# Performance work log

Measured on AMD Instinct MI355X. Metric: run time of the kernel, lower is better.

## Reference

```python
import jax, jax.numpy as jnp
import numpy as np

N = 50000; E = 800000; H = 4; C = 64; FEAT = 128; EDIM = 16; G = 256
NEG_SLOPE = 0.2; BN_EPS = 1e-5


def _gat_layer(x, src, dst, W, a_src, a_dst, bias, gamma, beta, alpha_edge=None):
    # GATConv (concat=True, PyG math), then BatchNorm1d (batch stats) + ReLU.
    h = (x @ W).reshape(N, H, C)                       # [N,H,C]
    alpha = (h * a_src).sum(-1)[src] + (h * a_dst).sum(-1)[dst]   # [Etot,H]
    if alpha_edge is not None:
        alpha = alpha + alpha_edge
    alpha = jax.nn.leaky_relu(alpha, NEG_SLOPE)
    amax = jax.ops.segment_max(alpha, dst, num_segments=N)        # edge softmax over dst
    ea = jnp.exp(alpha - amax[dst])
    denom = jax.ops.segment_sum(ea, dst, num_segments=N)
    coef = ea / (denom[dst] + 1e-16)
    out = jax.ops.segment_sum(coef[:, :, None] * h[src], dst, num_segments=N)
    out = out.reshape(N, H * C) + bias
    mu = out.mean(0)
    var = out.var(0)
    out = (out - mu) / jnp.sqrt(var + BN_EPS) * gamma + beta
    return jax.nn.relu(out)


def setup_inputs() -> dict:
    key = jax.random.key(0)
    ks = jax.random.split(key, 32)
    s = 0.05
    inp = {
        "x": jax.random.normal(ks[0], (N, FEAT), jnp.float32),
        "edge_index": jax.random.randint(ks[1], (2, E), 0, N),
        "edge_attr": jax.random.normal(ks[2], (E, EDIM), jnp.float32),
        "batch": jnp.sort(jax.random.randint(ks[3], (N,), 0, G)),
    }
    in_dims = [FEAT, H * C, H * C]
    for i in range(3):
        k = 4 + 7 * i
        inp[f"W{i}"] = jax.random.normal(ks[k], (in_dims[i], H * C), jnp.float32) * s
        inp[f"att_src{i}"] = jax.random.normal(ks[k + 1], (H, C), jnp.float32) * s
        inp[f"att_dst{i}"] = jax.random.normal(ks[k + 2], (H, C), jnp.float32) * s
        inp[f"bias{i}"] = jnp.zeros((H * C,), jnp.float32)
        inp[f"gamma{i}"] = jnp.ones((H * C,), jnp.float32)
        inp[f"beta{i}"] = jnp.zeros((H * C,), jnp.float32)
    inp["We0"] = jax.random.normal(ks[28], (EDIM, H * C), jnp.float32) * s
    inp["att_e0"] = jax.random.normal(ks[29], (H, C), jnp.float32) * s
    return inp


def reference(x, edge_index, edge_attr, batch,
              W0, att_src0, att_dst0, bias0, gamma0, beta0,
              W1, att_src1, att_dst1, bias1, gamma1, beta1,
              W2, att_src2, att_dst2, bias2, gamma2, beta2,
              We0, att_e0):
    # PyG GATConv adds self-loops; edge_attr for self-loops filled with mean.
    loops = jnp.arange(N)
    src = jnp.concatenate([edge_index[0], loops])
    dst = jnp.concatenate([edge_index[1], loops])
    ea_sl = jnp.concatenate([edge_attr, jnp.broadcast_to(edge_attr.mean(0), (N, EDIM))], 0)
    e = (ea_sl @ We0).reshape(E + N, H, C)
    alpha_e = (e * att_e0).sum(-1)                     # [Etot,H]
    x = _gat_layer(x, src, dst, W0, att_src0, att_dst0, bias0, gamma0, beta0, alpha_e)
    x = _gat_layer(x, src, dst, W1, att_src1, att_dst1, bias1, gamma1, beta1)
    x = _gat_layer(x, src, dst, W2, att_src2, att_dst2, bias2, gamma2, beta2)
    # global_mean_pool
    counts = jax.ops.segment_sum(jnp.ones((N,), x.dtype), batch, num_segments=G)
    sums = jax.ops.segment_sum(x, batch, num_segments=G)
    return sums / jnp.clip(counts, 1.0)[:, None]
```

## Files before the change

### kernel.cpp

```cpp
#include <hip/hip_runtime.h>
#include <math.h>

#define NN 50000
#define NE 800000
#define ET 850000
#define HCC 256
#define GG 256
#define CAP 64
#define NB 16

constexpr int RTILES = 782;
constexpr int G0B    = 512;
constexpr int CSRB   = 416;

constexpr size_t NHC    = (size_t)NN * HCC;
constexpr size_t O_H    = 0;
constexpr size_t O_AGG  = O_H + NHC / 2;
constexpr size_t O_REC  = O_AGG + NHC / 2;
constexpr size_t O_BT0  = O_REC + (size_t)NN * CAP * 4;
constexpr size_t O_BT1  = O_BT0 + 16384;
constexpr size_t O_BT2  = O_BT1 + 32768;
constexpr size_t O_AS   = O_BT2 + 32768;
constexpr size_t O_AD   = O_AS + (size_t)NN * 4;
constexpr size_t O_M    = O_AD + (size_t)NN * 4;
constexpr size_t O_ZERO = O_M + 64;
constexpr size_t O_DEG  = O_ZERO;
constexpr size_t O_SLS  = O_DEG + NN;
constexpr size_t O_PART = O_SLS + 4;
constexpr size_t O_END  = O_PART + 3 * NB * 512;
constexpr size_t ZWORDS = O_END - O_ZERO;
constexpr int    ZBLK   = (int)((ZWORDS / 4 + 255) / 256);
constexpr int    XBLK   = (int)((size_t)NN * 128 / 2048);

typedef __attribute__((ext_vector_type(8))) short bf16x8;
typedef __attribute__((ext_vector_type(4))) float f32x4;

__device__ inline unsigned short f2bf(float f) {
    unsigned int u = __float_as_uint(f);
    unsigned int r = (u + 0x7fffu + ((u >> 16) & 1u)) >> 16;
    return (unsigned short)r;
}
__device__ inline float b2f(unsigned short u) {
    return __uint_as_float(((unsigned int)u) << 16);
}
__device__ inline float bflo(unsigned int u) { return __uint_as_float(u << 16); }
__device__ inline float bfhi(unsigned int u) { return __uint_as_float(u & 0xffff0000u); }

__global__ void prep_kernel(const float* __restrict__ W0, const float* __restrict__ W1,
                            const float* __restrict__ W2,
                            const float* __restrict__ We0, const float* __restrict__ att_e0,
                            unsigned short* __restrict__ Bt0,
                            unsigned short* __restrict__ Bt1,
                            unsigned short* __restrict__ Bt2,
                            float* __restrict__ M, float* __restrict__ zbase,
                            const float* __restrict__ x, unsigned short* __restrict__ xb) {
    int b = blockIdx.x;
    if (b >= 641 + ZBLK) {
        size_t i0 = ((size_t)(b - (641 + ZBLK)) * 256 + threadIdx.x) * 8;
        float4 f1 = *(const float4*)(x + i0);
        float4 f2 = *(const float4*)(x + i0 + 4);
        uint4 o;
        o.x = ((unsigned)f2bf(f1.y) << 16) | f2bf(f1.x);
        o.y = ((unsigned)f2bf(f1.w) << 16) | f2bf(f1.z);
        o.z = ((unsigned)f2bf(f2.y) << 16) | f2bf(f2.x);
        o.w = ((unsigned)f2bf(f2.w) << 16) | f2bf(f2.z);
        *(uint4*)(xb + i0) = o;
        return;
    }
    if (b >= 641) {
        size_t idx = ((size_t)(b - 641) * 256 + threadIdx.x) * 4;
        if (idx < ZWORDS)
            *(float4*)(zbase + idx) = make_float4(0.f, 0.f, 0.f, 0.f);
        return;
    }
    if (b == 640) {
        int t = threadIdx.x;
        if (t < 64) {
            int k = t >> 2, hh = t & 3;
            float s = 0.f;
            for (int c = 0; c < 64; ++c)
                s += We0[k * 256 + hh * 64 + c] * att_e0[hh * 64 + c];
            M[k * 4 + hh] = s;
        }
        return;
    }
    const float* W; unsigned short* Bt; int K, base;
    if (b < 128)      { W = W0; Bt = Bt0; K = 128; base = 0; }
    else if (b < 384) { W = W1; Bt = Bt1; K = 256; base = 128; }
    else              { W = W2; Bt = Bt2; K = 256; base = 384; }
    int idx = (b - base) * 256 + threadIdx.x;
    int n = idx & 255, k = idx >> 8;
    Bt[(size_t)n * K + k] = f2bf(W[(size_t)k * 256 + n]);
}

__global__ __launch_bounds__(512) void g0csr(const unsigned short* __restrict__ Ab,
                                             const unsigned short* __restrict__ Bt,
                                             const float* __restrict__ att_src,
                                             const float* __restrict__ att_dst,
                                             unsigned short* __restrict__ Hout,
                                             float* __restrict__ asA,
                                             float* __restrict__ adA,
                                             const int* __restrict__ srcA,
                                             const int* __restrict__ dstA,
                                             const float* __restrict__ ea,
                                             const float* __restrict__ Mm,
                                             int* __restrict__ deg,
                                             uint4* __restrict__ rec,
                                             float* __restrict__ slsum) {
    constexpr int K   = 128;
    constexpr int KP  = K + 8;
    constexpr int NLD = K / 64;
    __shared__ unsigned short Bs[128][KP];
    __shared__ unsigned short As[2][64][KP];
    __shared__ float prt[8][4];

    int tid = threadIdx.x;
    int wave = tid >> 6, lane = tid & 63;

    if (blockIdx.x >= G0B) {
        int t0 = (int)(blockIdx.x - G0B) * 2048 + tid;
        float a0 = 0.f, a1 = 0.f, a2 = 0.f, a3 = 0.f;
        #pragma unroll
        for (int q = 0; q < 4; ++q) {
            int e = t0 + q * 512;
            if (e < ET) {
                bool real = (e < NE);
                int d = real ? dstA[e] : (e - NE);
                int s = real ? srcA[e] : (e - NE);
                int p = atomicAdd(&deg[d], 1);
                if (p > CAP - 1) p = CAP - 1;
                int slot = d * CAP + p;
                uint4 r;
                r.z = (unsigned)s;
                if (real) {
                    r.w = 0u;
                    const float4* pp = (const float4*)(ea + (size_t)e * 16);
                    float4 va = pp[0], vb = pp[1], vc = pp[2], vd = pp[3];
                    float v[16] = {va.x, va.y, va.z, va.w, vb.x, vb.y, vb.z, vb.w,
                                   vc.x, vc.y, vc.z, vc.w, vd.x, vd.y, vd.z, vd.w};
                    float o0 = 0.f, o1 = 0.f, o2 = 0.f, o3 = 0.f;
                    #pragma unroll
                    for (int k = 0; k < 16; ++k) {
                        float4 m4 = *(const float4*)(Mm + k * 4);
                        o0 = fmaf(v[k], m4.x, o0);
                        o1 = fmaf(v[k], m4.y, o1);
                        o2 = fmaf(v[k], m4.z, o2);
                        o3 = fmaf(v[k], m4.w, o3);
                    }
                    r.x = ((unsigned)f2bf(o1) << 16) | (unsigned)f2bf(o0);
                    r.y = ((unsigned)f2bf(o3) << 16) | (unsigned)f2bf(o2);
                    a0 += o0; a1 += o1; a2 += o2; a3 += o3;
                } else {
                    r.x = 0u; r.y = 0u; r.w = 1u;
                }
                rec[slot] = r;
            }
        }
        #pragma unroll
        for (int off = 32; off; off >>= 1) {
            a0 += __shfl_xor(a0, off);
            a1 += __shfl_xor(a1, off);
            a2 += __shfl_xor(a2, off);
            a3 += __shfl_xor(a3, off);
        }
        if (lane == 0) {
            prt[wave][0] = a0; prt[wave][1] = a1;
            prt[wave][2] = a2; prt[wave][3] = a3;
        }
        __syncthreads();
        if (tid < 4) {
            float s = 0.f;
            #pragma unroll
            for (int w = 0; w < 8; ++w) s += prt[w][tid];
            atomicAdd(&slsum[tid], s);
        }
        return;
    }

    int quad = lane >> 4, l16 = lane & 15;
    int wr = wave >> 1, wc = wave & 1;

    int b = blockIdx.x;
    int cb = (b >> 3) & 1;
    int ts = ((b >> 4) << 3) | (b & 7);
    const int np = G0B >> 1;
    int colbase = cb * 128;
    int head = cb * 2 + wc;

    {
        constexpr int TOT = 128 * K;
        for (int idx = tid * 8; idx < TOT; idx += 4096) {
            int br = idx / K, bk = idx % K;
            uint4 v = *(const uint4*)(Bt + (size_t)(colbase + br) * K + bk);
            *(uint4*)&Bs[br][bk] = v;
        }
    }

    int srow = tid >> 3;
    const int scol0 = (tid & 7) * (K / 8);

    uint4 ldA_[NLD], ldB_[NLD];

    auto issue = [&](uint4 (&ld)[NLD], int t) {
        int r = t * 64 + srow;
        if (r < NN) {
            const uint4* src = (const uint4*)(Ab + (size_t)r * K + scol0);
            #pragma unroll
            for (int q = 0; q < NLD; ++q) ld[q] = src[q];
        } else {
            #pragma unroll
            for (int q = 0; q < NLD; ++q) ld[q] = make_uint4(0u, 0u, 0u, 0u);
        }
    };
    auto commit = [&](uint4 (&ld)[NLD], int buf) {
        #pragma unroll
        for (int q = 0; q < NLD; ++q)
            *(uint4*)&As[buf][srow][scol0 + q * 8] = ld[q];
    };

    float asc[4], adc_[4];
    #pragma unroll
    for (int ni = 0; ni < 4; ++ni) {
        int c = colbase + wc * 64 + ni * 16 + l16;
        asc[ni]  = att_src[c];
        adc_[ni] = att_dst[c];
    }

    __syncthreads();

    auto tilestep = [&](uint4 (&ldCur)[NLD], uint4 (&ldNxt)[NLD], int buf, int t, int tn) {
        if (tn < RTILES) issue(ldNxt, tn);
        commit(ldCur, buf);
        __syncthreads();

        f32x4 acc[4] = {};
        #pragma unroll
        for (int k0 = 0; k0 < K; k0 += 32) {
            bf16x8 af, bfr[4];
            af = *(const bf16x8*)&As[buf][wr * 16 + l16][k0 + quad * 8];
            #pragma unroll
            for (int ni = 0; ni < 4; ++ni)
                bfr[ni] = *(const bf16x8*)&Bs[wc * 64 + ni * 16 + l16][k0 + quad * 8];
            #pragma unroll
            for (int ni = 0; ni < 4; ++ni)
                acc[ni] = __builtin_amdgcn_mfma_f32_16x16x32_bf16(
                    af, bfr[ni], acc[ni], 0, 0, 0);
        }
        int row0 = t * 64 + wr * 16;
        #pragma unroll
        for (int reg = 0; reg < 4; ++reg) {
            int r = row0 + quad * 4 + reg;
            if (r < NN) {
                #pragma unroll
                for (int ni = 0; ni < 4; ++ni) {
                    int c = colbase + wc * 64 + ni * 16 + l16;
                    Hout[(size_t)r * HCC + c] = f2bf(acc[ni][reg]);
                }
            }
            float s1 = acc[0][reg] * asc[0] + acc[1][reg] * asc[1] +
                       acc[2][reg] * asc[2] + acc[3][reg] * asc[3];
            float d1 = acc[0][reg] * adc_[0] + acc[1][reg] * adc_[1] +
                       acc[2][reg] * adc_[2] + acc[3][reg] * adc_[3];
            #pragma unroll
            for (int off = 1; off < 16; off <<= 1) {
                s1 += __shfl_xor(s1, off);
                d1 += __shfl_xor(d1, off);
            }
            if (l16 == 0 && r < NN) {
                asA[(size_t)r * 4 + head] = s1;
                adA[(size_t)r * 4 + head] = d1;
            }
        }
    };

    int t = ts;
    issue(ldA_, t);
    while (t < RTILES) {
        int t1 = t + np;
        tilestep(ldA_, ldB_, 0, t, t1);
        t = t1;
        if (t >= RTILES) break;
        int t2 = t + np;
        tilestep(ldB_, ldA_, 1, t, t2);
        t = t2;
    }
}

template <int K, bool NORM>
__global__ __launch_bounds__(512) void gemm2(const unsigned short* __restrict__ Ab,
                                             const unsigned short* __restrict__ Bt,
                                             const float* __restrict__ part,
                                             const float* __restrict__ gamma,
                                             const float* __restrict__ beta,
                                             const float* __restrict__ att_src,
                                             const float* __restrict__ att_dst,
                                             unsigned short* __restrict__ Hout,
                                             float* __restrict__ asA,
                                             float* __restrict__ adA, int M) {
    constexpr int KP  = K + 8;
    constexpr int NLD = K / 64;
    __shared__ unsigned short Bs[128][KP];
    __shared__ unsigned short As[2][64][KP];
    __shared__ float kvs[256], cvs[256];

    int tid = threadIdx.x;
    int wave = tid >> 6, lane = tid & 63;
    int quad = lane >> 4, l16 = lane & 15;
    int wr = wave >> 1, wc = wave & 1;

    int b = blockIdx.x;
    int cb = (b >> 3) & 1;
    int ts = ((b >> 4) << 3) | (b & 7);
    int np = (int)(gridDim.x >> 1);
    int colbase = cb * 128;
    int head = cb * 2 + wc;

    if (NORM) {
        if (tid < 256) {
            int ch = tid;
            float s = 0.f, s2 = 0.f;
            #pragma unroll
            for (int q = 0; q < NB; ++q) {
                s  += part[q * 512 + ch];
                s2 += part[q * 512 + 256 + ch];
            }
            const float invN = 1.0f / (float)NN;
            float mr = s * invN;
            float var = s2 * invN - mr * mr;
            float k = gamma[ch] * rsqrtf(var + 1e-5f);
            kvs[ch] = k;
            cvs[ch] = beta[ch] - mr * k;
        }
    }
    {
        constexpr int TOT = 128 * K;
        for (int idx = tid * 8; idx < TOT; idx += 4096) {
            int br = idx / K, bk = idx % K;
            uint4 v = *(const uint4*)(Bt + (size_t)(colbase + br) * K + bk);
            *(uint4*)&Bs[br][bk] = v;
        }
    }

    int srow = tid >> 3;
    const int scol0 = (tid & 7) * (K / 8);

    uint4 ldA_[NLD], ldB_[NLD];

    auto issue = [&](uint4 (&ld)[NLD], int t) {
        int r = t * 64 + srow;
        if (r < M) {
            const uint4* src = (const uint4*)(Ab + (size_t)r * K + scol0);
            #pragma unroll
            for (int q = 0; q < NLD; ++q) ld[q] = src[q];
        } else {
            #pragma unroll
            for (int q = 0; q < NLD; ++q) ld[q] = make_uint4(0u, 0u, 0u, 0u);
        }
    };
    auto commit = [&](uint4 (&ld)[NLD], int buf) {
        #pragma unroll
        for (int q = 0; q < NLD; ++q) {
            uint4 v = ld[q];
            if (NORM) {
                int ch = scol0 + q * 8;
                float u[8] = {bflo(v.x), bfhi(v.x), bflo(v.y), bfhi(v.y),
                              bflo(v.z), bfhi(v.z), bflo(v.w), bfhi(v.w)};
                #pragma unroll
                for (int j = 0; j < 8; ++j)
                    u[j] = fmaxf(fmaf(u[j], kvs[ch + j], cvs[ch + j]), 0.f);
                v.x = ((unsigned)f2bf(u[1]) << 16) | f2bf(u[0]);
                v.y = ((unsigned)f2bf(u[3]) << 16) | f2bf(u[2]);
                v.z = ((unsigned)f2bf(u[5]) << 16) | f2bf(u[4]);
                v.w = ((unsigned)f2bf(u[7]) << 16) | f2bf(u[6]);
            }
            *(uint4*)&As[buf][srow][scol0 + q * 8] = v;
        }
    };

    float asc[4], adc_[4];
    #pragma unroll
    for (int ni = 0; ni < 4; ++ni) {
        int c = colbase + wc * 64 + ni * 16 + l16;
        asc[ni]  = att_src[c];
        adc_[ni] = att_dst[c];
    }

    __syncthreads();

    auto tilestep = [&](uint4 (&ldCur)[NLD], uint4 (&ldNxt)[NLD], int buf, int t, int tn) {
        if (tn < RTILES) issue(ldNxt, tn);
        commit(ldCur, buf);
        __syncthreads();
        f32x4 acc[4] = {};
        #pragma unroll
        for (int k0 = 0; k0 < K; k0 += 32) {
            bf16x8 af, bfr[4];
            af = *(const bf16x8*)&As[buf][wr * 16 + l16][k0 + quad * 8];
            #pragma unroll
            for (int ni = 0; ni < 4; ++ni)
                bfr[ni] = *(const bf16x8*)&Bs[wc * 64 + ni * 16 + l16][k0 + quad * 8];
            #pragma unroll
            for (int ni = 0; ni < 4; ++ni)
                acc[ni] = __builtin_amdgcn_mfma_f32_16x16x32_bf16(
                    af, bfr[ni], acc[ni], 0, 0, 0);
        }
        int row0 = t * 64 + wr * 16;
        #pragma unroll
        for (int reg = 0; reg < 4; ++reg) {
            int r = row0 + quad * 4 + reg;
            if (r < M) {
                #pragma unroll
                for (int ni = 0; ni < 4; ++ni) {
                    int c = colbase + wc * 64 + ni * 16 + l16;
                    Hout[(size_t)r * HCC + c] = f2bf(acc[ni][reg]);
                }
            }
            float s1 = acc[0][reg] * asc[0] + acc[1][reg] * asc[1] +
                       acc[2][reg] * asc[2] + acc[3][reg] * asc[3];
            float d1 = acc[0][reg] * adc_[0] + acc[1][reg] * adc_[1] +
                       acc[2][reg] * adc_[2] + acc[3][reg] * adc_[3];
            #pragma unroll
            for (int off = 1; off < 16; off <<= 1) {
                s1 += __shfl_xor(s1, off);
                d1 += __shfl_xor(d1, off);
            }
            if (l16 == 0 && r < M) {
                asA[(size_t)r * 4 + head] = s1;
                adA[(size_t)r * 4 + head] = d1;
            }
        }
    };

    int t = ts;
    issue(ldA_, t);
    while (t < RTILES) {
        int t1 = t + np;
        tilestep(ldA_, ldB_, 0, t, t1);
        t = t1;
        if (t >= RTILES) break;
        int t2 = t + np;
        tilestep(ldB_, ldA_, 1, t, t2);
        t = t2;
    }
}

template <bool HAS_AE>
__global__ __launch_bounds__(256) void agg_kernel(const unsigned short* __restrict__ Hm,
                                                  const float* __restrict__ asA,
                                                  const float* __restrict__ adA,
                                                  const uint4* __restrict__ rec,
                                                  const int* __restrict__ degA,
                                                  const float* __restrict__ slsum,
                                                  unsigned short* __restrict__ outA,
                                                  float* __restrict__ part) {
    __shared__ float wlds[4][260];
    __shared__ float slds[2][4][256];
    int wave = threadIdx.x >> 6, lane = threadIdx.x & 63;
    int n = blockIdx.x * 4 + wave;
    int head = lane >> 4;
    int st = n * CAP;
    int d = degA[n];
    if (d > CAP) d = CAP;
    float4 ad4 = *(const float4*)(adA + (size_t)n * 4);

    float4 w4 = make_float4(0.f, 0.f, 0.f, 0.f);
    int ms = 0;
    if (lane < d) {
        uint4 r = rec[st + lane];
        ms = (int)r.z;
        float4 av = *(const float4*)(asA + (size_t)ms * 4);
        float4 t = make_float4(av.x + ad4.x, av.y + ad4.y, av.z + ad4.z, av.w + ad4.w);
        if (HAS_AE) {
            if (r.w) {
                const float inv = 1.0f / (float)NE;
                t.x += slsum[0] * inv; t.y += slsum[1] * inv;
                t.z += slsum[2] * inv; t.w += slsum[3] * inv;
            } else {
                t.x += bflo(r.x); t.y += bfhi(r.x);
                t.z += bflo(r.y); t.w += bfhi(r.y);
            }
        }
        t.x = (t.x > 0.f) ? t.x : 0.2f * t.x;
        t.y = (t.y > 0.f) ? t.y : 0.2f * t.y;
        t.z = (t.z > 0.f) ? t.z : 0.2f * t.z;
        t.w = (t.w > 0.f) ? t.w : 0.2f * t.w;
        w4.x = __expf(t.x);
        w4.y = __expf(t.y);
        w4.z = __expf(t.z);
        w4.w = __expf(t.w);
    }
    float4 Dv = w4;
    wlds[wave][0 * 65 + lane] = w4.x;
    wlds[wave][1 * 65 + lane] = w4.y;
    wlds[wave][2 * 65 + lane] = w4.z;
    wlds[wave][3 * 65 + lane] = w4.w;

    float4 acc = make_float4(0.f, 0.f, 0.f, 0.f);
    const unsigned short* hb = Hm + lane * 4;
    int cnt8 = (d + 7) & ~7;
    const float* wrow = &wlds[wave][head * 65];

    int sj0[8], sj1[8];
    ushort4 hv0[8], hv1[8];
    #pragma unroll
    for (int q = 0; q < 8; ++q)
        sj0[q] = __builtin_amdgcn_readlane(ms, q);
    #pragma unroll
    for (int q = 0; q < 8; ++q)
        hv0[q] = *(const ushort4*)(hb + (size_t)sj0[q] * HCC);
    if (cnt8 > 8) {
        #pragma unroll
        for (int q = 0; q < 8; ++q)
            sj1[q] = __builtin_amdgcn_readlane(ms, 8 + q);
        #pragma unroll
        for (int q = 0; q < 8; ++q)
            hv1[q] = *(const ushort4*)(hb + (size_t)sj1[q] * HCC);
    }
    for (int jj = 0; jj < cnt8; jj += 16) {
        {
            float wq[8];
            #pragma unroll
            for (int q = 0; q < 8; ++q)
                wq[q] = wrow[jj + q];
            #pragma unroll
            for (int q = 0; q < 8; ++q) {
                acc.x = fmaf(wq[q], b2f(hv0[q].x), acc.x);
                acc.y = fmaf(wq[q], b2f(hv0[q].y), acc.y);
                acc.z = fmaf(wq[q], b2f(hv0[q].z), acc.z);
                acc.w = fmaf(wq[q], b2f(hv0[q].w), acc.w);
            }
            if (jj + 16 < cnt8) {
                #pragma unroll
                for (int q = 0; q < 8; ++q)
                    sj0[q] = __builtin_amdgcn_readlane(ms, jj + 16 + q);
                #pragma unroll
                for (int q = 0; q < 8; ++q)
                    hv0[q] = *(const ushort4*)(hb + (size_t)sj0[q] * HCC);
            }
        }
        if (jj + 8 < cnt8) {
            float wq[8];
            #pragma unroll
            for (int q = 0; q < 8; ++q)
                wq[q] = wrow[jj + 8 + q];
            #pragma unroll
            for (int q = 0; q < 8; ++q) {
                acc.x = fmaf(wq[q], b2f(hv1[q].x), acc.x);
                acc.y = fmaf(wq[q], b2f(hv1[q].y), acc.y);
                acc.z = fmaf(wq[q], b2f(hv1[q].z), acc.z);
                acc.w = fmaf(wq[q], b2f(hv1[q].w), acc.w);
            }
            if (jj + 24 < cnt8) {
                #pragma unroll
                for (int q = 0; q < 8; ++q)
                    sj1[q] = __builtin_amdgcn_readlane(ms, jj + 24 + q);
                #pragma unroll
                for (int q = 0; q < 8; ++q)
                    hv1[q] = *(const ushort4*)(hb + (size_t)sj1[q] * HCC);
            }
        }
    }
    #pragma unroll
    for (int off = 32; off; off >>= 1) {
        Dv.x += __shfl_xor(Dv.x, off);
        Dv.y += __shfl_xor(Dv.y, off);
        Dv.z += __shfl_xor(Dv.z, off);
        Dv.w += __shfl_xor(Dv.w, off);
    }
    float D = (head & 2) ? ((head & 1) ? Dv.w : Dv.z) : ((head & 1) ? Dv.y : Dv.x);
    float inv = 1.0f / (D + 1e-16f);
    float4 o = make_float4(acc.x * inv, acc.y * inv, acc.z * inv, acc.w * inv);
    ushort4 ob = make_ushort4(f2bf(o.x), f2bf(o.y), f2bf(o.z), f2bf(o.w));
    *(ushort4*)(outA + (size_t)n * HCC + lane * 4) = ob;

    *(float4*)&slds[0][wave][lane * 4] = o;
    *(float4*)&slds[1][wave][lane * 4] =
        make_float4(o.x * o.x, o.y * o.y, o.z * o.z, o.w * o.w);
    __syncthreads();
    {
        int ch = threadIdx.x;
        float s0 = 0.f, s1 = 0.f;
        #pragma unroll
        for (int w = 0; w < 4; ++w) {
            s0 += slds[0][w][ch];
            s1 += slds[1][w][ch];
        }
        int bucket = blockIdx.x & (NB - 1);
        atomicAdd(&part[bucket * 512 + ch], s0);
        atomicAdd(&part[bucket * 512 + 256 + ch], s1);
    }
}

__global__ void pool_kernel(const unsigned short* __restrict__ aggb,
                            const float* __restrict__ part,
                            const float* __restrict__ gamma, const float* __restrict__ beta,
                            const int* __restrict__ batch,
                            float* __restrict__ out) {
    int ch = threadIdx.x;
    int g = blockIdx.x;
    float s = 0.f, s2 = 0.f;
    #pragma unroll
    for (int b = 0; b < NB; ++b) {
        s  += part[b * 512 + ch];
        s2 += part[b * 512 + 256 + ch];
    }
    const float invN = 1.0f / (float)NN;
    float mr = s * invN;
    float var = s2 * invN - mr * mr;
    float k = gamma[ch] * rsqrtf(var + 1e-5f);
    float c = beta[ch] - mr * k;

    int lo = 0, hi = NN;
    while (lo < hi) { int mid = (lo + hi) >> 1; if (batch[mid] < g) lo = mid + 1; else hi = mid; }
    int start = lo;
    lo = start; hi = NN;
    while (lo < hi) { int mid = (lo + hi) >> 1; if (batch[mid] < g + 1) lo = mid + 1; else hi = mid; }
    int end = lo;

    float a0 = 0.f, a1 = 0.f, a2 = 0.f, a3 = 0.f;
    int n = start;
    for (; n + 3 < end; n += 4) {
        a0 += fmaxf(fmaf(b2f(aggb[(size_t)n * HCC + ch]), k, c), 0.f);
        a1 += fmaxf(fmaf(b2f(aggb[(size_t)(n + 1) * HCC + ch]), k, c), 0.f);
        a2 += fmaxf(fmaf(b2f(aggb[(size_t)(n + 2) * HCC + ch]), k, c), 0.f);
        a3 += fmaxf(fmaf(b2f(aggb[(size_t)(n + 3) * HCC + ch]), k, c), 0.f);
    }
    for (; n < end; ++n)
        a0 += fmaxf(fmaf(b2f(aggb[(size_t)n * HCC + ch]), k, c), 0.f);
    float tot = (a0 + a1) + (a2 + a3);
    out[(size_t)g * HCC + ch] = tot / fmaxf((float)(end - start), 1.0f);
}

extern "C" void kernel_launch(void* const* d_in, const int* in_sizes, int n_in,
                              void* d_out, int out_size, void* d_ws, size_t ws_size,
                              hipStream_t stream) {
    const float* x = (const float*)d_in[0];
    const int* edge_index = (const int*)d_in[1];
    const int* srcA = edge_index;
    const int* dstA = edge_index + NE;
    const float* edge_attr = (const float*)d_in[2];
    const int* batch = (const int*)d_in[3];
    const float* W[3]   = {(const float*)d_in[4],  (const float*)d_in[10], (const float*)d_in[16]};
    const float* asc[3] = {(const float*)d_in[5],  (const float*)d_in[11], (const float*)d_in[17]};
    const float* adc[3] = {(const float*)d_in[6],  (const float*)d_in[12], (const float*)d_in[18]};
    const float* gam[3] = {(const float*)d_in[8],  (const float*)d_in[14], (const float*)d_in[20]};
    const float* bet[3] = {(const float*)d_in[9],  (const float*)d_in[15], (const float*)d_in[21]};
    const float* We0 = (const float*)d_in[22];
    const float* att_e0 = (const float*)d_in[23];

    float* wsf = (float*)d_ws;
    unsigned short* hbuf = (unsigned short*)(wsf + O_H);
    unsigned short* aggb = (unsigned short*)(wsf + O_AGG);
    unsigned short* xb   = aggb;
    uint4* rec   = (uint4*)(wsf + O_REC);
    unsigned short* Bt0  = (unsigned short*)(wsf + O_BT0);
    unsigned short* Bt1  = (unsigned short*)(wsf + O_BT1);
    unsigned short* Bt2  = (unsigned short*)(wsf + O_BT2);
    float* asA   = wsf + O_AS;
    float* adA   = wsf + O_AD;
    float* Mb    = wsf + O_M;
    int*   deg   = (int*)(wsf + O_DEG);
    float* slsum = wsf + O_SLS;
    float* part  = wsf + O_PART;

    prep_kernel<<<641 + ZBLK + XBLK, 256, 0, stream>>>(W[0], W[1], W[2], We0, att_e0,
                                                       Bt0, Bt1, Bt2, Mb, wsf + O_ZERO,
                                                       x, xb);

    g0csr<<<G0B + CSRB, 512, 0, stream>>>(xb, Bt0, asc[0], adc[0], hbuf, asA, adA,
                                          srcA, dstA, edge_attr, Mb, deg, rec, slsum);
    agg_kernel<true><<<12500, 256, 0, stream>>>(hbuf, asA, adA, rec, deg, slsum,
        aggb, part + (size_t)0 * NB * 512);

    gemm2<256, true><<<256, 512, 0, stream>>>(aggb, Bt1, part + (size_t)0 * NB * 512,
        gam[0], bet[0], asc[1], adc[1], hbuf, asA, adA, NN);
    agg_kernel<false><<<12500, 256, 0, stream>>>(hbuf, asA, adA, rec, deg, slsum,
        aggb, part + (size_t)1 * NB * 512);

    gemm2<256, true><<<256, 512, 0, stream>>>(aggb, Bt2, part + (size_t)1 * NB * 512,
        gam[1], bet[1], asc[2], adc[2], hbuf, asA, adA, NN);
    agg_kernel<false><<<12500, 256, 0, stream>>>(hbuf, asA, adA, rec, deg, slsum,
        aggb, part + (size_t)2 * NB * 512);

    pool_kernel<<<GG, 256, 0, stream>>>(aggb, part + (size_t)2 * NB * 512,
                                        gam[2], bet[2], batch, (float*)d_out);
}
```

Measured before the change: 520.0 us.

## Fuse x bf16 conversion into GEMM0, widen agg blocks, simplify gather pipeline

```diff
diff --git a/kernel.cpp b/kernel.cpp
--- a/kernel.cpp
+++ b/kernel.cpp
@@ -30,7 +30,6 @@
 constexpr size_t O_END  = O_PART + 3 * NB * 512;
 constexpr size_t ZWORDS = O_END - O_ZERO;
 constexpr int    ZBLK   = (int)((ZWORDS / 4 + 255) / 256);
-constexpr int    XBLK   = (int)((size_t)NN * 128 / 2048);
 
 typedef __attribute__((ext_vector_type(8))) short bf16x8;
 typedef __attribute__((ext_vector_type(4))) float f32x4;
@@ -52,21 +51,8 @@
                             unsigned short* __restrict__ Bt0,
                             unsigned short* __restrict__ Bt1,
                             unsigned short* __restrict__ Bt2,
-                            float* __restrict__ M, float* __restrict__ zbase,
-                            const float* __restrict__ x, unsigned short* __restrict__ xb) {
+                            float* __restrict__ M, float* __restrict__ zbase) {
     int b = blockIdx.x;
-    if (b >= 641 + ZBLK) {
-        size_t i0 = ((size_t)(b - (641 + ZBLK)) * 256 + threadIdx.x) * 8;
-        float4 f1 = *(const float4*)(x + i0);
-        float4 f2 = *(const float4*)(x + i0 + 4);
-        uint4 o;
-        o.x = ((unsigned)f2bf(f1.y) << 16) | f2bf(f1.x);
-        o.y = ((unsigned)f2bf(f1.w) << 16) | f2bf(f1.z);
-        o.z = ((unsigned)f2bf(f2.y) << 16) | f2bf(f2.x);
-        o.w = ((unsigned)f2bf(f2.w) << 16) | f2bf(f2.z);
-        *(uint4*)(xb + i0) = o;
-        return;
-    }
     if (b >= 641) {
         size_t idx = ((size_t)(b - 641) * 256 + threadIdx.x) * 4;
         if (idx < ZWORDS)
@@ -93,7 +79,7 @@
     Bt[(size_t)n * K + k] = f2bf(W[(size_t)k * 256 + n]);
 }
 
-__global__ __launch_bounds__(512) void g0csr(const unsigned short* __restrict__ Ab,
+__global__ __launch_bounds__(512) void g0csr(const float* __restrict__ xf,
                                              const unsigned short* __restrict__ Bt,
                                              const float* __restrict__ att_src,
                                              const float* __restrict__ att_dst,
@@ -107,9 +93,8 @@
                                              int* __restrict__ deg,
                                              uint4* __restrict__ rec,
                                              float* __restrict__ slsum) {
-    constexpr int K   = 128;
-    constexpr int KP  = K + 8;
-    constexpr int NLD = K / 64;
+    constexpr int K  = 128;
+    constexpr int KP = K + 8;
     __shared__ unsigned short Bs[128][KP];
     __shared__ unsigned short As[2][64][KP];
     __shared__ float prt[8][4];
@@ -197,25 +182,32 @@
     }
 
     int srow = tid >> 3;
-    const int scol0 = (tid & 7) * (K / 8);
-
-    uint4 ldA_[NLD], ldB_[NLD];
-
-    auto issue = [&](uint4 (&ld)[NLD], int t) {
+    const int scol0 = (tid & 7) * 16;
+
+    float4 ldA_[4], ldB_[4];
+
+    auto issue = [&](float4 (&ld)[4], int t) {
         int r = t * 64 + srow;
         if (r < NN) {
-            const uint4* src = (const uint4*)(Ab + (size_t)r * K + scol0);
-            #pragma unroll
-            for (int q = 0; q < NLD; ++q) ld[q] = src[q];
+            const float4* src = (const float4*)(xf + (size_t)r * K + scol0);
+            #pragma unroll
+            for (int q = 0; q < 4; ++q) ld[q] = src[q];
         } else {
             #pragma unroll
-            for (int q = 0; q < NLD; ++q) ld[q] = make_uint4(0u, 0u, 0u, 0u);
+            for (int q = 0; q < 4; ++q) ld[q] = make_float4(0.f, 0.f, 0.f, 0.f);
         }
     };
-    auto commit = [&](uint4 (&ld)[NLD], int buf) {
-        #pragma unroll
-        for (int q = 0; q < NLD; ++q)
-            *(uint4*)&As[buf][srow][scol0 + q * 8] = ld[q];
+    auto commit = [&](float4 (&ld)[4], int buf) {
+        #pragma unroll
+        for (int q = 0; q < 2; ++q) {
+            float4 a = ld[2 * q], c = ld[2 * q + 1];
+            uint4 v;
+            v.x = ((unsigned)f2bf(a.y) << 16) | f2bf(a.x);
+            v.y = ((unsigned)f2bf(a.w) << 16) | f2bf(a.z);
+            v.z = ((unsigned)f2bf(c.y) << 16) | f2bf(c.x);
+            v.w = ((unsigned)f2bf(c.w) << 16) | f2bf(c.z);
+            *(uint4*)&As[buf][srow][scol0 + q * 8] = v;
+        }
     };
 
     float asc[4], adc_[4];
@@ -226,12 +218,16 @@
         adc_[ni] = att_dst[c];
     }
 
-    __syncthreads();
-
-    auto tilestep = [&](uint4 (&ldCur)[NLD], uint4 (&ldNxt)[NLD], int buf, int t, int tn) {
+    int t = ts;
+    issue(ldA_, t);
+    asm volatile("s_waitcnt lgkmcnt(0)" ::: "memory");
+    __builtin_amdgcn_s_barrier();
+
+    auto tilestep = [&](float4 (&ldCur)[4], float4 (&ldNxt)[4], int buf, int t_, int tn) {
         if (tn < RTILES) issue(ldNxt, tn);
         commit(ldCur, buf);
-        __syncthreads();
+        asm volatile("s_waitcnt lgkmcnt(0)" ::: "memory");
+        __builtin_amdgcn_s_barrier();
 
         f32x4 acc[4] = {};
         #pragma unroll
@@ -246,7 +242,7 @@
                 acc[ni] = __builtin_amdgcn_mfma_f32_16x16x32_bf16(
                     af, bfr[ni], acc[ni], 0, 0, 0);
         }
-        int row0 = t * 64 + wr * 16;
+        int row0 = t_ * 64 + wr * 16;
         #pragma unroll
         for (int reg = 0; reg < 4; ++reg) {
             int r = row0 + quad * 4 + reg;
@@ -273,8 +269,6 @@
         }
     };
 
-    int t = ts;
-    issue(ldA_, t);
     while (t < RTILES) {
         int t1 = t + np;
         tilestep(ldA_, ldB_, 0, t, t1);
@@ -385,12 +379,17 @@
         adc_[ni] = att_dst[c];
     }
 
-    __syncthreads();
-
-    auto tilestep = [&](uint4 (&ldCur)[NLD], uint4 (&ldNxt)[NLD], int buf, int t, int tn) {
+    int t = ts;
+    issue(ldA_, t);
+    asm volatile("s_waitcnt lgkmcnt(0)" ::: "memory");
+    __builtin_amdgcn_s_barrier();
+
+    auto tilestep = [&](uint4 (&ldCur)[NLD], uint4 (&ldNxt)[NLD], int buf, int t_, int tn) {
         if (tn < RTILES) issue(ldNxt, tn);
         commit(ldCur, buf);
-        __syncthreads();
+        asm volatile("s_waitcnt lgkmcnt(0)" ::: "memory");
+        __builtin_amdgcn_s_barrier();
+
         f32x4 acc[4] = {};
         #pragma unroll
         for (int k0 = 0; k0 < K; k0 += 32) {
@@ -404,7 +403,7 @@
                 acc[ni] = __builtin_amdgcn_mfma_f32_16x16x32_bf16(
                     af, bfr[ni], acc[ni], 0, 0, 0);
         }
-        int row0 = t * 64 + wr * 16;
+        int row0 = t_ * 64 + wr * 16;
         #pragma unroll
         for (int reg = 0; reg < 4; ++reg) {
             int r = row0 + quad * 4 + reg;
@@ -431,8 +430,6 @@
         }
     };
 
-    int t = ts;
-    issue(ldA_, t);
     while (t < RTILES) {
         int t1 = t + np;
         tilestep(ldA_, ldB_, 0, t, t1);
@@ -445,7 +442,7 @@
 }
 
 template <bool HAS_AE>
-__global__ __launch_bounds__(256) void agg_kernel(const unsigned short* __restrict__ Hm,
+__global__ __launch_bounds__(512) void agg_kernel(const unsigned short* __restrict__ Hm,
                                                   const float* __restrict__ asA,
                                                   const float* __restrict__ adA,
                                                   const uint4* __restrict__ rec,
@@ -453,10 +450,10 @@
                                                   const float* __restrict__ slsum,
                                                   unsigned short* __restrict__ outA,
                                                   float* __restrict__ part) {
-    __shared__ float wlds[4][260];
-    __shared__ float slds[2][4][256];
+    __shared__ float wlds[8][260];
+    __shared__ float slds[2][8][256];
     int wave = threadIdx.x >> 6, lane = threadIdx.x & 63;
-    int n = blockIdx.x * 4 + wave;
+    int n = blockIdx.x * 8 + wave;
     int head = lane >> 4;
     int st = n * CAP;
     int d = degA[n];
@@ -500,64 +497,41 @@
     int cnt8 = (d + 7) & ~7;
     const float* wrow = &wlds[wave][head * 65];
 
-    int sj0[8], sj1[8];
-    ushort4 hv0[8], hv1[8];
+    int sjA[8]; ushort4 hvA[8];
     #pragma unroll
     for (int q = 0; q < 8; ++q)
-        sj0[q] = __builtin_amdgcn_readlane(ms, q);
+        sjA[q] = __builtin_amdgcn_readlane(ms, q);
     #pragma unroll
     for (int q = 0; q < 8; ++q)
-        hv0[q] = *(const ushort4*)(hb + (size_t)sj0[q] * HCC);
-    if (cnt8 > 8) {
+        hvA[q] = *(const ushort4*)(hb + (size_t)sjA[q] * HCC);
+    for (int jj = 0; jj < cnt8; jj += 8) {
+        int nj = jj + 8;
+        bool more = (nj < cnt8);
+        ushort4 hvB[8];
+        if (more) {
+            int sjB[8];
+            #pragma unroll
+            for (int q = 0; q < 8; ++q)
+                sjB[q] = __builtin_amdgcn_readlane(ms, nj + q);
+            #pragma unroll
+            for (int q = 0; q < 8; ++q)
+                hvB[q] = *(const ushort4*)(hb + (size_t)sjB[q] * HCC);
+        }
+        float wq[8];
         #pragma unroll
         for (int q = 0; q < 8; ++q)
-            sj1[q] = __builtin_amdgcn_readlane(ms, 8 + q);
-        #pragma unroll
-        for (int q = 0; q < 8; ++q)
-            hv1[q] = *(const ushort4*)(hb + (size_t)sj1[q] * HCC);
-    }
-    for (int jj = 0; jj < cnt8; jj += 16) {
-        {
-            float wq[8];
+            wq[q] = wrow[jj + q];
+        #pragma unroll
+        for (int q = 0; q < 8; ++q) {
+            acc.x = fmaf(wq[q], b2f(hvA[q].x), acc.x);
+            acc.y = fmaf(wq[q], b2f(hvA[q].y), acc.y);
+            acc.z = fmaf(wq[q], b2f(hvA[q].z), acc.z);
+            acc.w = fmaf(wq[q], b2f(hvA[q].w), acc.w);
+        }
+        if (more) {
             #pragma unroll
             for (int q = 0; q < 8; ++q)
-                wq[q] = wrow[jj + q];
-            #pragma unroll
-            for (int q = 0; q < 8; ++q) {
-                acc.x = fmaf(wq[q], b2f(hv0[q].x), acc.x);
-                acc.y = fmaf(wq[q], b2f(hv0[q].y), acc.y);
-                acc.z = fmaf(wq[q], b2f(hv0[q].z), acc.z);
-                acc.w = fmaf(wq[q], b2f(hv0[q].w), acc.w);
-            }
-            if (jj + 16 < cnt8) {
-                #pragma unroll
-                for (int q = 0; q < 8; ++q)
-                    sj0[q] = __builtin_amdgcn_readlane(ms, jj + 16 + q);
-                #pragma unroll
-                for (int q = 0; q < 8; ++q)
-                    hv0[q] = *(const ushort4*)(hb + (size_t)sj0[q] * HCC);
-            }
-        }
-        if (jj + 8 < cnt8) {
-            float wq[8];
-            #pragma unroll
-            for (int q = 0; q < 8; ++q)
-                wq[q] = wrow[jj + 8 + q];
-            #pragma unroll
-            for (int q = 0; q < 8; ++q) {
-                acc.x = fmaf(wq[q], b2f(hv1[q].x), acc.x);
-                acc.y = fmaf(wq[q], b2f(hv1[q].y), acc.y);
-                acc.z = fmaf(wq[q], b2f(hv1[q].z), acc.z);
-                acc.w = fmaf(wq[q], b2f(hv1[q].w), acc.w);
-            }
-            if (jj + 24 < cnt8) {
-                #pragma unroll
-                for (int q = 0; q < 8; ++q)
-                    sj1[q] = __builtin_amdgcn_readlane(ms, jj + 24 + q);
-                #pragma unroll
-                for (int q = 0; q < 8; ++q)
-                    hv1[q] = *(const ushort4*)(hb + (size_t)sj1[q] * HCC);
-            }
+                hvA[q] = hvB[q];
         }
     }
     #pragma unroll
@@ -577,17 +551,15 @@
     *(float4*)&slds[1][wave][lane * 4] =
         make_float4(o.x * o.x, o.y * o.y, o.z * o.z, o.w * o.w);
     __syncthreads();
-    {
-        int ch = threadIdx.x;
-        float s0 = 0.f, s1 = 0.f;
-        #pragma unroll
-        for (int w = 0; w < 4; ++w) {
-            s0 += slds[0][w][ch];
-            s1 += slds[1][w][ch];
-        }
+    int t = threadIdx.x;
+    if (t < 512) {
+        int ch = t & 255, which = t >> 8;
+        float s = 0.f;
+        #pragma unroll
+        for (int w = 0; w < 8; ++w)
+            s += slds[which][w][ch];
         int bucket = blockIdx.x & (NB - 1);
-        atomicAdd(&part[bucket * 512 + ch], s0);
-        atomicAdd(&part[bucket * 512 + 256 + ch], s1);
+        atomicAdd(&part[bucket * 512 + which * 256 + ch], s);
     }
 }
 
@@ -651,7 +623,6 @@
     float* wsf = (float*)d_ws;
     unsigned short* hbuf = (unsigned short*)(wsf + O_H);
     unsigned short* aggb = (unsigned short*)(wsf + O_AGG);
-    unsigned short* xb   = aggb;
     uint4* rec   = (uint4*)(wsf + O_REC);
     unsigned short* Bt0  = (unsigned short*)(wsf + O_BT0);
     unsigned short* Bt1  = (unsigned short*)(wsf + O_BT1);
@@ -663,23 +634,22 @@
     float* slsum = wsf + O_SLS;
     float* part  = wsf + O_PART;
 
-    prep_kernel<<<641 + ZBLK + XBLK, 256, 0, stream>>>(W[0], W[1], W[2], We0, att_e0,
-                                                       Bt0, Bt1, Bt2, Mb, wsf + O_ZERO,
-                                                       x, xb);
-
-    g0csr<<<G0B + CSRB, 512, 0, stream>>>(xb, Bt0, asc[0], adc[0], hbuf, asA, adA,
+    prep_kernel<<<641 + ZBLK, 256, 0, stream>>>(W[0], W[1], W[2], We0, att_e0,
+                                                Bt0, Bt1, Bt2, Mb, wsf + O_ZERO);
+
+    g0csr<<<G0B + CSRB, 512, 0, stream>>>(x, Bt0, asc[0], adc[0], hbuf, asA, adA,
                                           srcA, dstA, edge_attr, Mb, deg, rec, slsum);
-    agg_kernel<true><<<12500, 256, 0, stream>>>(hbuf, asA, adA, rec, deg, slsum,
+    agg_kernel<true><<<6250, 512, 0, stream>>>(hbuf, asA, adA, rec, deg, slsum,
         aggb, part + (size_t)0 * NB * 512);
 
     gemm2<256, true><<<256, 512, 0, stream>>>(aggb, Bt1, part + (size_t)0 * NB * 512,
         gam[0], bet[0], asc[1], adc[1], hbuf, asA, adA, NN);
-    agg_kernel<false><<<12500, 256, 0, stream>>>(hbuf, asA, adA, rec, deg, slsum,
+    agg_kernel<false><<<6250, 512, 0, stream>>>(hbuf, asA, adA, rec, deg, slsum,
         aggb, part + (size_t)1 * NB * 512);
 
     gemm2<256, true><<<256, 512, 0, stream>>>(aggb, Bt2, part + (size_t)1 * NB * 512,
         gam[1], bet[1], asc[2], adc[2], hbuf, asA, adA, NN);
-    agg_kernel<false><<<12500, 256, 0, stream>>>(hbuf, asA, adA, rec, deg, slsum,
+    agg_kernel<false><<<6250, 512, 0, stream>>>(hbuf, asA, adA, rec, deg, slsum,
         aggb, part + (size_t)2 * NB * 512);
 
     pool_kernel<<<GG, 256, 0, stream>>>(aggb, part + (size_t)2 * NB * 512,
```

Result: faster. 494.6 us (-4.9%).
